# Kernel optimization log

Hardware: AMD Instinct MI355X
Metric: run time of the kernel (lower is better)

## Reference

```python
import jax, jax.numpy as jnp
import numpy as np

NUM_NODES = 50000
NUM_EDGES = 640000
H_DIM = 128
OUT_DIM = 128
NUM_RELS = 16
NUM_BASES = 8


def _rgcn_layer(h, basis, coef, bias, src, dst, etype, norm, activation):
    # Basis decomposition: W[r] = sum_b coef[r,b] * basis[b]  -> [R, d_in, d_out]
    W = jnp.einsum('rb,bio->rio', coef, basis)
    # Transform node features under every relation: [R, N, d_out]
    Hr = jnp.einsum('ni,rio->rno', h, W)
    # Per-edge message: pick (relation, source) pair, apply edge norm. [E, d_out]
    msg = Hr[etype, src] * norm
    # Aggregate messages at destination nodes. [N, d_out]
    out = jax.ops.segment_sum(msg, dst, num_segments=h.shape[0])
    out = out + bias
    return activation(out) if activation is not None else out


def setup_inputs() -> dict:
    key = jax.random.key(0)
    ks = jax.random.split(key, 10)
    h = jax.random.normal(ks[0], (NUM_NODES, H_DIM), dtype=jnp.float32)
    norm = jax.random.uniform(ks[1], (NUM_EDGES, 1), dtype=jnp.float32)
    src = jax.random.randint(ks[2], (NUM_EDGES,), 0, NUM_NODES, dtype=jnp.int32)
    dst = jax.random.randint(ks[3], (NUM_EDGES,), 0, NUM_NODES, dtype=jnp.int32)
    etype = jax.random.randint(ks[4], (NUM_EDGES,), 0, NUM_RELS, dtype=jnp.int32)
    s1 = 1.0 / np.sqrt(H_DIM)
    s2 = 1.0 / np.sqrt(H_DIM)
    V1 = jax.random.normal(ks[5], (NUM_BASES, H_DIM, H_DIM), dtype=jnp.float32) * s1
    coef1 = jax.random.normal(ks[6], (NUM_RELS, NUM_BASES), dtype=jnp.float32) * (1.0 / np.sqrt(NUM_BASES))
    bias1 = jnp.zeros((H_DIM,), dtype=jnp.float32)
    V2 = jax.random.normal(ks[7], (NUM_BASES, H_DIM, OUT_DIM), dtype=jnp.float32) * s2
    coef2 = jax.random.normal(ks[8], (NUM_RELS, NUM_BASES), dtype=jnp.float32) * (1.0 / np.sqrt(NUM_BASES))
    bias2 = jnp.zeros((OUT_DIM,), dtype=jnp.float32)
    return {
        'h': h, 'norm': norm, 'src': src, 'dst': dst, 'etype': etype,
        'V1': V1, 'coef1': coef1, 'bias1': bias1,
        'V2': V2, 'coef2': coef2, 'bias2': bias2,
    }


def reference(h, norm, src, dst, etype, V1, coef1, bias1, V2, coef2, bias2):
    # Layer 0: relational graph conv with ReLU (hidden layer)
    h1 = _rgcn_layer(h, V1, coef1, bias1, src, dst, etype, norm, jax.nn.relu)
    # Layer 1+: BaseRGCN sorts edges by relation (bucketing for the low-mem
    # per-relation dispatch). The sort is a permutation of the edge set, so we
    # mirror it explicitly; the segment_sum result is mathematically identical.
    order = jnp.argsort(etype)
    src_s, dst_s, et_s, norm_s = src[order], dst[order], etype[order], norm[order]
    out = _rgcn_layer(h1, V2, coef2, bias2, src_s, dst_s, et_s, norm_s, None)
    return out
```

## Files before the change

### kernel.cpp

```cpp
#include <hip/hip_runtime.h>

#define N_RELS 16
#define N_BASES 8
#define HD 128
#define SCAN_B 1024
#define ROWS 32

typedef __attribute__((ext_vector_type(8))) short bf16x8;
typedef __attribute__((ext_vector_type(4))) float floatx4;
typedef __attribute__((ext_vector_type(2))) float floatx2;

__device__ __forceinline__ short bf16rn(float f) {
    union { float f; unsigned u; } v; v.f = f;
    unsigned u = v.u;
    unsigned r = (u + 0x7fffu + ((u >> 16) & 1u)) >> 16;
    return (short)r;
}


__global__ void setup_fused(const float* __restrict__ h, unsigned* __restrict__ hb, int n2,
                            const float* __restrict__ V1, const float* __restrict__ V2,
                            short* __restrict__ Vf,
                            const int* __restrict__ dst, int E, int* __restrict__ cnt,
                            int packBlocks, int vBlocks) {
    int blk = blockIdx.x;
    if (blk < packBlocks) {
        int i = blk * blockDim.x + threadIdx.x;
        if (i < n2) {
            float2 v = ((const float2*)h)[i];
            hb[i] = ((unsigned)(unsigned short)bf16rn(v.y) << 16) | (unsigned short)bf16rn(v.x);
        }
        return;
    }
    blk -= packBlocks;
    if (blk < vBlocks) {
        const float* V = ((blk & 8) ? V2 : V1) + (size_t)(blk & 7) * 16384;
        size_t obase = (size_t)blk * 16384;
        for (int e = threadIdx.x; e < 16384; e += blockDim.x) {
            float w = V[e];
            int k = e >> 7, n = e & 127;
            int kk = k >> 5, q = (k >> 3) & 3, j = k & 7;
            int lane = q * 16 + (n & 15);
            int idx = ((kk * 8 + (n >> 4)) * 64 + lane) * 8 + j;
            Vf[obase + idx] = bf16rn(w);
        }
        return;
    }
    blk -= vBlocks;
    int i = blk * blockDim.x + threadIdx.x;
    if (i < E) atomicAdd(&cnt[dst[i]], 1);
}


__global__ void scan_partial(const int* __restrict__ cnt, int N,
                             int* __restrict__ excl, int* __restrict__ bsum) {
    __shared__ int s[SCAN_B];
    int t = threadIdx.x, i = blockIdx.x * SCAN_B + t;
    int v = (i < N) ? cnt[i] : 0;
    s[t] = v; __syncthreads();
    for (int o = 1; o < SCAN_B; o <<= 1) {
        int x = (t >= o) ? s[t - o] : 0;
        __syncthreads();
        s[t] += x;
        __syncthreads();
    }
    if (i < N) excl[i] = s[t] - v;
    if (t == SCAN_B - 1) bsum[blockIdx.x] = s[t];
}

__global__ void scan_fixup(int* __restrict__ row_ptr, const int* __restrict__ bsum,
                           int nb, int N, int E, int* __restrict__ cursor) {
    __shared__ int pref[64];
    int t = threadIdx.x;
    if (t < 64) {
        int raw = (t < nb) ? bsum[t] : 0;
        int v = raw;
#pragma unroll
        for (int o = 1; o < 64; o <<= 1) {
            int u = __shfl_up(v, o, 64);
            if (t >= o) v += u;
        }
        pref[t] = v - raw;
    }
    __syncthreads();
    int i = blockIdx.x * blockDim.x + t;
    if (i < N) { int val = row_ptr[i] + pref[i >> 10]; row_ptr[i] = val; cursor[i] = val; }
    if (i == 0) row_ptr[N] = E;
}

__global__ void scatter_dst(const int* __restrict__ dst, const int* __restrict__ src,
                            const int* __restrict__ et, const float* __restrict__ norm,
                            int E, int* __restrict__ cursor, int2* __restrict__ edata) {
    int i = blockIdx.x * blockDim.x + threadIdx.x;
    if (i >= E) return;
    int p = atomicAdd(&cursor[dst[i]], 1);
    edata[p] = make_int2((et[i] << 16) | src[i], __float_as_int(norm[i]));
}


__global__ __launch_bounds__(512, 4) void rgcn_tile(
    const unsigned* __restrict__ hb, const int2* __restrict__ edata,
    const int* __restrict__ row_ptr, const float* __restrict__ coef,
    const short* __restrict__ Vf, const float* __restrict__ bias,
    void* __restrict__ outp, int N, int mode) {
    __shared__ __align__(16) unsigned Zs[N_BASES][4][4][ROWS + 1][4];
    __shared__ int ticket;

    const int tid = threadIdx.x;
    const int wave = tid >> 6, lane = tid & 63;
    const int nb0 = blockIdx.x * ROWS;

    if (tid == 0) ticket = 0;
    __syncthreads();

    const int lkk = lane >> 4, lq = (lane >> 2) & 3, lju = lane & 3;

    for (;;) {
        int row0 = 0;
        if (lane == 0) row0 = atomicAdd(&ticket, 1);
        const int row = __builtin_amdgcn_readfirstlane(row0);
        if (row >= ROWS) break;
        const int node = nb0 + row;
        int e = 0, end = 0;
        if (node < N) { e = row_ptr[node]; end = row_ptr[node + 1]; }

        floatx2 acc[N_BASES] = {};
        auto proc = [&](int2 m, unsigned g) {
            int ets = __builtin_amdgcn_readfirstlane(m.x >> 16);
            float nv = __int_as_float(m.y);
            const float* cw = coef + ets * N_BASES;
            floatx2 v;
            v.x = __uint_as_float(g << 16) * nv;
            v.y = __uint_as_float(g & 0xffff0000u) * nv;
#pragma unroll
            for (int b = 0; b < N_BASES; b++)
                acc[b] = v * cw[b] + acc[b];
        };

        for (; e + 4 <= end; e += 4) {
            int2 m0 = edata[e], m1 = edata[e + 1], m2 = edata[e + 2], m3 = edata[e + 3];
            unsigned g0 = hb[(size_t)(m0.x & 0xffff) * 64 + lane];
            unsigned g1 = hb[(size_t)(m1.x & 0xffff) * 64 + lane];
            unsigned g2 = hb[(size_t)(m2.x & 0xffff) * 64 + lane];
            unsigned g3 = hb[(size_t)(m3.x & 0xffff) * 64 + lane];
            proc(m0, g0); proc(m1, g1); proc(m2, g2); proc(m3, g3);
        }
        for (; e < end; e++) {
            int2 m = edata[e];
            unsigned g = hb[(size_t)(m.x & 0xffff) * 64 + lane];
            proc(m, g);
        }

#pragma unroll
        for (int b = 0; b < N_BASES; b++) {
            unsigned lo = (unsigned)(unsigned short)bf16rn(acc[b].x);
            unsigned hi = (unsigned)(unsigned short)bf16rn(acc[b].y);
            Zs[b][lkk][lq][row][lju] = (hi << 16) | lo;
        }
    }
    __syncthreads();

    const int q = lane >> 4, cc = lane & 15;
    const int tt = wave;
    floatx4 ac0 = {}, ac1 = {};

#pragma unroll 2
    for (int b = 0; b < N_BASES; b++) {
#pragma unroll
        for (int kk = 0; kk < 4; kk++) {
            bf16x8 a0 = *(const bf16x8*)&Zs[b][kk][q][cc][0];
            bf16x8 a1 = *(const bf16x8*)&Zs[b][kk][q][16 + cc][0];
            bf16x8 B = *(const bf16x8*)(Vf + (size_t)b * 16384 +
                                        ((size_t)(kk * 8 + tt) * 64 + lane) * 8);
            ac0 = __builtin_amdgcn_mfma_f32_16x16x32_bf16(a0, B, ac0, 0, 0, 0);
            ac1 = __builtin_amdgcn_mfma_f32_16x16x32_bf16(a1, B, ac1, 0, 0, 0);
        }
    }

    float bv = bias[tt * 16 + cc];
    if (mode == 0) {
        unsigned short* o = (unsigned short*)outp;
#pragma unroll
        for (int mi = 0; mi < 2; mi++) {
            const floatx4& c = mi ? ac1 : ac0;
#pragma unroll
            for (int i = 0; i < 4; i++) {
                int node = nb0 + mi * 16 + q * 4 + i;
                if (node < N) {
                    float v = fmaxf(c[i] + bv, 0.f);
                    o[(size_t)node * HD + tt * 16 + cc] = (unsigned short)bf16rn(v);
                }
            }
        }
    } else {
        float* o = (float*)outp;
#pragma unroll
        for (int mi = 0; mi < 2; mi++) {
            const floatx4& c = mi ? ac1 : ac0;
#pragma unroll
            for (int i = 0; i < 4; i++) {
                int node = nb0 + mi * 16 + q * 4 + i;
                if (node < N) o[(size_t)node * HD + tt * 16 + cc] = c[i] + bv;
            }
        }
    }
}


extern "C" void kernel_launch(void* const* d_in, const int* in_sizes, int n_in,
                              void* d_out, int out_size, void* d_ws, size_t ws_size,
                              hipStream_t stream) {
    const float* h     = (const float*)d_in[0];
    const float* norm  = (const float*)d_in[1];
    const int*   src   = (const int*)d_in[2];
    const int*   dst   = (const int*)d_in[3];
    const int*   etype = (const int*)d_in[4];
    const float* V1    = (const float*)d_in[5];
    const float* coef1 = (const float*)d_in[6];
    const float* bias1 = (const float*)d_in[7];
    const float* V2    = (const float*)d_in[8];
    const float* coef2 = (const float*)d_in[9];
    const float* bias2 = (const float*)d_in[10];
    const int N = in_sizes[0] / HD;
    const int E = in_sizes[2];
    float* out = (float*)d_out;
    (void)n_in; (void)out_size; (void)ws_size;

    char* ws = (char*)d_ws;
    size_t off = 0;
    auto alloc = [&](size_t bytes) {
        void* p = ws + off;
        off += (bytes + 255) & ~(size_t)255;
        return p;
    };
    short*    Vf      = (short*)alloc((size_t)16 * 16384 * sizeof(short));
    unsigned* hb      = (unsigned*)alloc((size_t)N * 64 * sizeof(unsigned));
    unsigned* h1b     = (unsigned*)alloc((size_t)N * 64 * sizeof(unsigned));
    int2*     edata   = (int2*)alloc((size_t)E * sizeof(int2));
    int*      cnt     = (int*)alloc((size_t)N * sizeof(int));
    int*      row_ptr = (int*)alloc((size_t)(N + 1) * sizeof(int));
    int*      cursor  = (int*)alloc((size_t)N * sizeof(int));
    int*      bsum    = (int*)alloc(256 * sizeof(int));

    const int nb = (N + SCAN_B - 1) / SCAN_B;
    const int packBlocks = (N * 64 + 255) / 256;
    const int vBlocks = 16;
    const int histBlocks = (E + 255) / 256;

    hipMemsetAsync(cnt, 0, (size_t)N * sizeof(int), stream);
    setup_fused<<<packBlocks + vBlocks + histBlocks, 256, 0, stream>>>(
        h, hb, N * 64, V1, V2, Vf, dst, E, cnt, packBlocks, vBlocks);
    scan_partial<<<nb, SCAN_B, 0, stream>>>(cnt, N, row_ptr, bsum);
    scan_fixup<<<(N + 255) / 256, 256, 0, stream>>>(row_ptr, bsum, nb, N, E, cursor);
    scatter_dst<<<(E + 255) / 256, 256, 0, stream>>>(dst, src, etype, norm, E, cursor, edata);

    const int tiles = (N + ROWS - 1) / ROWS;

    rgcn_tile<<<tiles, 512, 0, stream>>>(hb, edata, row_ptr, coef1, Vf, bias1, h1b, N, 0);
    rgcn_tile<<<tiles, 512, 0, stream>>>(h1b, edata, row_ptr, coef2, Vf + (size_t)8 * 16384,
                                         bias2, out, N, 1);
}
```

Baseline: 322.3 us.

## Assign four contiguous rows per wave and software-pipeline edge metadata loads

The gather phase drops the shared-memory ticket atomic that dealt out rows dynamically. Each wave now owns four consecutive destination rows and walks their combined edge range as one stream, flushing the accumulators at each row boundary. Edge records are prefetched eight ahead in a double buffer, with indices clamped to stay in bounds, so more source-row gathers are in flight and the latency of the small per-row loops is hidden. Separately, the bf16 packing of h is vectorised to float4 loads. The tradeoff is static load balance: waves whose rows have higher degree can leave others idle.

Result: slower. 329.0 us (+2.1%).

```diff
diff --git a/kernel.cpp b/kernel.cpp
--- a/kernel.cpp
+++ b/kernel.cpp
@@ -18,7 +18,7 @@
 }
 
 
-__global__ void setup_fused(const float* __restrict__ h, unsigned* __restrict__ hb, int n2,
+__global__ void setup_fused(const float* __restrict__ h, unsigned* __restrict__ hb, int n4,
                             const float* __restrict__ V1, const float* __restrict__ V2,
                             short* __restrict__ Vf,
                             const int* __restrict__ dst, int E, int* __restrict__ cnt,
@@ -26,9 +26,12 @@
     int blk = blockIdx.x;
     if (blk < packBlocks) {
         int i = blk * blockDim.x + threadIdx.x;
-        if (i < n2) {
-            float2 v = ((const float2*)h)[i];
-            hb[i] = ((unsigned)(unsigned short)bf16rn(v.y) << 16) | (unsigned short)bf16rn(v.x);
+        if (i < n4) {
+            float4 v = ((const float4*)h)[i];
+            uint2 o;
+            o.x = ((unsigned)(unsigned short)bf16rn(v.y) << 16) | (unsigned short)bf16rn(v.x);
+            o.y = ((unsigned)(unsigned short)bf16rn(v.w) << 16) | (unsigned short)bf16rn(v.z);
+            ((uint2*)hb)[i] = o;
         }
         return;
     }
@@ -102,62 +105,84 @@
     const unsigned* __restrict__ hb, const int2* __restrict__ edata,
     const int* __restrict__ row_ptr, const float* __restrict__ coef,
     const short* __restrict__ Vf, const float* __restrict__ bias,
-    void* __restrict__ outp, int N, int mode) {
+    void* __restrict__ outp, int N, int E, int mode) {
     __shared__ __align__(16) unsigned Zs[N_BASES][4][4][ROWS + 1][4];
-    __shared__ int ticket;
 
     const int tid = threadIdx.x;
     const int wave = tid >> 6, lane = tid & 63;
     const int nb0 = blockIdx.x * ROWS;
 
-    if (tid == 0) ticket = 0;
-    __syncthreads();
-
     const int lkk = lane >> 4, lq = (lane >> 2) & 3, lju = lane & 3;
 
-    for (;;) {
-        int row0 = 0;
-        if (lane == 0) row0 = atomicAdd(&ticket, 1);
-        const int row = __builtin_amdgcn_readfirstlane(row0);
-        if (row >= ROWS) break;
-        const int node = nb0 + row;
-        int e = 0, end = 0;
-        if (node < N) { e = row_ptr[node]; end = row_ptr[node + 1]; }
-
-        floatx2 acc[N_BASES] = {};
-        auto proc = [&](int2 m, unsigned g) {
-            int ets = __builtin_amdgcn_readfirstlane(m.x >> 16);
-            float nv = __int_as_float(m.y);
-            const float* cw = coef + ets * N_BASES;
-            floatx2 v;
-            v.x = __uint_as_float(g << 16) * nv;
-            v.y = __uint_as_float(g & 0xffff0000u) * nv;
-#pragma unroll
-            for (int b = 0; b < N_BASES; b++)
-                acc[b] = v * cw[b] + acc[b];
-        };
-
-        for (; e + 4 <= end; e += 4) {
-            int2 m0 = edata[e], m1 = edata[e + 1], m2 = edata[e + 2], m3 = edata[e + 3];
-            unsigned g0 = hb[(size_t)(m0.x & 0xffff) * 64 + lane];
-            unsigned g1 = hb[(size_t)(m1.x & 0xffff) * 64 + lane];
-            unsigned g2 = hb[(size_t)(m2.x & 0xffff) * 64 + lane];
-            unsigned g3 = hb[(size_t)(m3.x & 0xffff) * 64 + lane];
-            proc(m0, g0); proc(m1, g1); proc(m2, g2); proc(m3, g3);
-        }
-        for (; e < end; e++) {
-            int2 m = edata[e];
-            unsigned g = hb[(size_t)(m.x & 0xffff) * 64 + lane];
-            proc(m, g);
-        }
-
+    const int r0 = wave * 4;
+    int bounds[5];
+#pragma unroll
+    for (int i = 0; i < 5; i++) {
+        int nd = nb0 + r0 + i; if (nd > N) nd = N;
+        bounds[i] = __builtin_amdgcn_readfirstlane(row_ptr[nd]);
+    }
+    int e = bounds[0];
+    const int eend = bounds[4];
+
+    floatx2 acc[N_BASES] = {};
+    int cur = 0;
+
+    auto proc = [&](int2 m, unsigned g) {
+        int ets = __builtin_amdgcn_readfirstlane(m.x >> 16);
+        float nv = __int_as_float(m.y);
+        const float* cw = coef + ets * N_BASES;
+        floatx2 v;
+        v.x = __uint_as_float(g << 16) * nv;
+        v.y = __uint_as_float(g & 0xffff0000u) * nv;
+#pragma unroll
+        for (int b = 0; b < N_BASES; b++)
+            acc[b] = v * cw[b] + acc[b];
+    };
+    auto flush = [&](int r) {
 #pragma unroll
         for (int b = 0; b < N_BASES; b++) {
             unsigned lo = (unsigned)(unsigned short)bf16rn(acc[b].x);
             unsigned hi = (unsigned)(unsigned short)bf16rn(acc[b].y);
-            Zs[b][lkk][lq][row][lju] = (hi << 16) | lo;
-        }
-    }
+            Zs[b][lkk][lq][r0 + r][lju] = (hi << 16) | lo;
+            acc[b].x = 0.f; acc[b].y = 0.f;
+        }
+    };
+
+    int2 mb[8];
+#pragma unroll
+    for (int j = 0; j < 8; j++) { int ix = e + j; if (ix > E - 1) ix = E - 1; mb[j] = edata[ix]; }
+
+    while (e + 8 <= eend) {
+        unsigned g[8];
+#pragma unroll
+        for (int j = 0; j < 8; j++) g[j] = hb[(size_t)(mb[j].x & 0xffff) * 64 + lane];
+        int2 nxt[8];
+#pragma unroll
+        for (int j = 0; j < 8; j++) { int ix = e + 8 + j; if (ix > E - 1) ix = E - 1; nxt[j] = edata[ix]; }
+#pragma unroll
+        for (int j = 0; j < 8; j++) {
+            while (cur < 3 && e + j >= bounds[cur + 1]) { flush(cur); cur++; }
+            proc(mb[j], g[j]);
+        }
+#pragma unroll
+        for (int j = 0; j < 8; j++) mb[j] = nxt[j];
+        e += 8;
+    }
+    {
+        const int rem = eend - e;
+        unsigned g[8];
+#pragma unroll
+        for (int j = 0; j < 8; j++)
+            if (j < rem) g[j] = hb[(size_t)(mb[j].x & 0xffff) * 64 + lane];
+#pragma unroll
+        for (int j = 0; j < 8; j++)
+            if (j < rem) {
+                while (cur < 3 && e + j >= bounds[cur + 1]) { flush(cur); cur++; }
+                proc(mb[j], g[j]);
+            }
+    }
+    while (cur < 4) { flush(cur); cur++; }
+
     __syncthreads();
 
     const int q = lane >> 4, cc = lane & 15;
@@ -243,20 +268,20 @@
     int*      bsum    = (int*)alloc(256 * sizeof(int));
 
     const int nb = (N + SCAN_B - 1) / SCAN_B;
-    const int packBlocks = (N * 64 + 255) / 256;
+    const int packBlocks = (N * 32 + 255) / 256;
     const int vBlocks = 16;
     const int histBlocks = (E + 255) / 256;
 
     hipMemsetAsync(cnt, 0, (size_t)N * sizeof(int), stream);
     setup_fused<<<packBlocks + vBlocks + histBlocks, 256, 0, stream>>>(
-        h, hb, N * 64, V1, V2, Vf, dst, E, cnt, packBlocks, vBlocks);
+        h, hb, N * 32, V1, V2, Vf, dst, E, cnt, packBlocks, vBlocks);
     scan_partial<<<nb, SCAN_B, 0, stream>>>(cnt, N, row_ptr, bsum);
     scan_fixup<<<(N + 255) / 256, 256, 0, stream>>>(row_ptr, bsum, nb, N, E, cursor);
     scatter_dst<<<(E + 255) / 256, 256, 0, stream>>>(dst, src, etype, norm, E, cursor, edata);
 
     const int tiles = (N + ROWS - 1) / ROWS;
 
-    rgcn_tile<<<tiles, 512, 0, stream>>>(hb, edata, row_ptr, coef1, Vf, bias1, h1b, N, 0);
+    rgcn_tile<<<tiles, 512, 0, stream>>>(hb, edata, row_ptr, coef1, Vf, bias1, h1b, N, E, 0);
     rgcn_tile<<<tiles, 512, 0, stream>>>(h1b, edata, row_ptr, coef2, Vf + (size_t)8 * 16384,
-                                         bias2, out, N, 1);
-}
+                                         bias2, out, N, E, 1);
+}
```
